# Performance work log

Hardware: AMD Instinct MI355X
Metric: run time of the kernel (lower is better)

## Reference

```python
import jax, jax.numpy as jnp
import numpy as np

D_MODEL = 512
N_HEADS = 8
D_FF = 2048
EPS = 1e-6


def layer_norm(x, g, b):
    mu = jnp.mean(x, axis=-1, keepdims=True)
    var = jnp.mean(jnp.square(x - mu), axis=-1, keepdims=True)
    return (x - mu) * jax.lax.rsqrt(var + EPS) * g + b


def setup_inputs() -> dict:
    key = jax.random.key(0)
    ks = jax.random.split(key, 6)
    B, S = 64, 500
    x = jax.random.normal(ks[0], (B, S, D_MODEL), dtype=jnp.float32)
    ln1_g = jnp.ones((D_MODEL,), jnp.float32)
    ln1_b = jnp.zeros((D_MODEL,), jnp.float32)
    ln2_g = jnp.ones((D_MODEL,), jnp.float32)
    ln2_b = jnp.zeros((D_MODEL,), jnp.float32)
    W1 = jax.random.normal(ks[1], (D_MODEL, D_FF), jnp.float32) * (1.0 / np.sqrt(D_MODEL))
    b1 = jnp.zeros((D_FF,), jnp.float32)
    W2 = jax.random.normal(ks[2], (D_FF, D_MODEL), jnp.float32) * (1.0 / np.sqrt(D_FF))
    b2 = jnp.zeros((D_MODEL,), jnp.float32)
    return {"x": x, "ln1_g": ln1_g, "ln1_b": ln1_b, "ln2_g": ln2_g, "ln2_b": ln2_b,
            "W1": W1, "b1": b1, "W2": W2, "b2": b2}


def causal_attention(h):
    # h: [B, S, D]; q=k=v=h (no projections in this module)
    B, S, D = h.shape
    Hd = D // N_HEADS
    qkv = h.reshape(B, S, N_HEADS, Hd).transpose(0, 2, 1, 3)  # [B, H, S, Hd]
    w = jnp.einsum('bhsd,bhtd->bhst', qkv, qkv) / jnp.sqrt(jnp.float32(Hd))
    mask = jnp.tril(jnp.ones((S, S), dtype=bool))
    w = jnp.where(mask, w, jnp.finfo(w.dtype).min)
    w = jax.nn.softmax(w, axis=-1)
    out = jnp.einsum('bhst,bhtd->bhsd', w, qkv)  # [B, H, S, Hd]
    return out.transpose(0, 2, 1, 3).reshape(B, S, D)


def reference(x, ln1_g, ln1_b, ln2_g, ln2_b, W1, b1, W2, b2):
    # Pre-LN block, but residuals attach to the post-LN activations (faithful to source).
    h = layer_norm(x, ln1_g, ln1_b)
    h = h + causal_attention(h)
    h2 = layer_norm(h, ln2_g, ln2_b)
    ff = jnp.maximum(h2 @ W1 + b1, 0.0) @ W2 + b2
    return h2 + ff
```

## Files before the change

kernel.cpp:

```cpp
#include <hip/hip_runtime.h>
#include <hip/hip_bf16.h>

#define D_MODEL 512
#define N_HEADS 8
#define HDIM 64
#define D_FF 2048
#define BATCH 64
#define SEQ 500
#define MROWS (BATCH * SEQ)

typedef __attribute__((ext_vector_type(8))) short bhalf8;
typedef __attribute__((ext_vector_type(4))) float floatx4;

#define AS_GLOBAL __attribute__((address_space(1)))
#define AS_LDS __attribute__((address_space(3)))

__device__ __forceinline__ void glds16(const void* g, void* l) {
  __builtin_amdgcn_global_load_lds((const AS_GLOBAL unsigned int*)g,
                                   (AS_LDS unsigned int*)l, 16, 0, 0);
}

__device__ __forceinline__ unsigned short f2bf(float f) {
  __hip_bfloat16 b = __float2bfloat16(f);
  return *reinterpret_cast<unsigned short*>(&b);
}

template <int MODE>
__global__ __launch_bounds__(256) void ln_kernel(const void* __restrict__ xin,
                                                 const float* __restrict__ g,
                                                 const float* __restrict__ b,
                                                 __hip_bfloat16* __restrict__ yb) {
  int row = blockIdx.x;
  int t = threadIdx.x;
  float v0, v1;
  if constexpr (MODE == 0) {
    float2 v = ((const float2*)xin)[(size_t)row * 256 + t];
    v0 = v.x; v1 = v.y;
  } else {
    __hip_bfloat162 bv = ((const __hip_bfloat162*)xin)[(size_t)row * 256 + t];
    v0 = __bfloat162float(bv.x); v1 = __bfloat162float(bv.y);
  }
  float s = v0 + v1;
  float sq = v0 * v0 + v1 * v1;
#pragma unroll
  for (int off = 32; off > 0; off >>= 1) {
    s += __shfl_down(s, off, 64);
    sq += __shfl_down(sq, off, 64);
  }
  __shared__ float red[8];
  if ((t & 63) == 0) {
    red[(t >> 6) * 2] = s;
    red[(t >> 6) * 2 + 1] = sq;
  }
  __syncthreads();
  s = red[0] + red[2] + red[4] + red[6];
  sq = red[1] + red[3] + red[5] + red[7];
  float mean = s * (1.0f / 512.0f);
  float var = sq * (1.0f / 512.0f) - mean * mean;
  float r = rsqrtf(var + 1e-6f);
  float2 gg = ((const float2*)g)[t];
  float2 bb = ((const float2*)b)[t];
  float y0 = (v0 - mean) * r * gg.x + bb.x;
  float y1 = (v1 - mean) * r * gg.y + bb.y;
  __hip_bfloat162 bv2;
  bv2.x = __float2bfloat16(y0);
  bv2.y = __float2bfloat16(y1);
  ((__hip_bfloat162*)yb)[(size_t)row * 256 + t] = bv2;
}

__global__ __launch_bounds__(256) void transpose_bf16(const float* __restrict__ W,
                                                      __hip_bfloat16* __restrict__ Wt,
                                                      int K, int N) {
  __shared__ float tile[32][33];
  int n0 = blockIdx.x * 32, k0 = blockIdx.y * 32;
  int tx = threadIdx.x, ty = threadIdx.y;
#pragma unroll
  for (int j = 0; j < 32; j += 8)
    tile[ty + j][tx] = W[(size_t)(k0 + ty + j) * N + n0 + tx];
  __syncthreads();
#pragma unroll
  for (int j = 0; j < 32; j += 8)
    Wt[(size_t)(n0 + ty + j) * K + k0 + tx] = __float2bfloat16(tile[tx][ty + j]);
}

__device__ __forceinline__ void attn_tile_step(int jq, int kt, int fr, int kg,
                                               const char* Kb, const char* Vb,
                                               char* Pw, bhalf8 (&qf)[2][2],
                                               floatx4 (&O)[2][4], float (&l)[2][4]) {
  int roff = 32 * jq - 64 * kt;
  bool domask = (jq <= 2 * kt + 1);
#pragma unroll
  for (int mr = 0; mr < 2; ++mr) {
    floatx4 S[4];
#pragma unroll
    for (int nc = 0; nc < 4; ++nc) S[nc] = (floatx4){0.f, 0.f, 0.f, 0.f};
    __builtin_amdgcn_s_setprio(1);
#pragma unroll
    for (int kk = 0; kk < 2; ++kk) {
#pragma unroll
      for (int nc = 0; nc < 4; ++nc) {
        bhalf8 kf = *(const bhalf8*)(Kb + (nc * 16 + fr) * 128 +
                                     (((kk * 4 + kg) ^ (fr & 7)) << 4));
        S[nc] = __builtin_amdgcn_mfma_f32_16x16x32_bf16(qf[mr][kk], kf, S[nc], 0, 0, 0);
      }
    }
    __builtin_amdgcn_s_setprio(0);
    if (domask) {
#pragma unroll
      for (int nc = 0; nc < 4; ++nc)
#pragma unroll
        for (int j = 0; j < 4; ++j)
          if (nc * 16 + fr > roff + mr * 16 + kg * 4 + j) S[nc][j] = -INFINITY;
    }
    float p[4][4];
#pragma unroll
    for (int nc = 0; nc < 4; ++nc)
#pragma unroll
      for (int j = 0; j < 4; ++j) {
        p[nc][j] = __expf(S[nc][j] * 0.125f - 66.0f);
        l[mr][j] += p[nc][j];
      }
#pragma unroll
    for (int nc = 0; nc < 4; ++nc)
#pragma unroll
      for (int j = 0; j < 4; ++j)
        *(unsigned short*)(Pw + ((kg * 4 + j) * 72 + nc * 16 + fr) * 2) = f2bf(p[nc][j]);
    __builtin_amdgcn_s_setprio(1);
#pragma unroll
    for (int kk = 0; kk < 2; ++kk) {
      bhalf8 pf = *(const bhalf8*)(Pw + fr * 144 + kk * 64 + kg * 16);
#pragma unroll
      for (int nc = 0; nc < 4; ++nc) {
        bhalf8 vf = *(const bhalf8*)(Vb + (nc * 16 + fr) * 144 + kk * 64 + kg * 16);
        O[mr][nc] = __builtin_amdgcn_mfma_f32_16x16x32_bf16(pf, vf, O[mr][nc], 0, 0, 0);
      }
    }
    __builtin_amdgcn_s_setprio(0);
  }
}

__global__ __launch_bounds__(512) void attn_fold(const __hip_bfloat16* __restrict__ hbp,
                                                 __hip_bfloat16* __restrict__ hres) {
  __shared__ unsigned short Ks[2][64 * 64];
  __shared__ unsigned short Vt[2][64 * 72];
  __shared__ unsigned short Ps[8][16 * 72];

  int blk = blockIdx.x;
  int b = blk >> 3, hd = blk & 7;
  int tid = threadIdx.x;
  int w = tid >> 6, lane = tid & 63;
  int fr = lane & 15, kg = lane >> 4;

  const unsigned short* hb = (const unsigned short*)hbp;
  size_t bbase = (size_t)b * SEQ * D_MODEL + hd * HDIM;

  int jH = 15 - w, jL = w;
  bhalf8 qH[2][2], qL[2][2];
#pragma unroll
  for (int mr = 0; mr < 2; ++mr) {
    int rH = 32 * jH + mr * 16 + fr;
    if (rH >= SEQ) rH = SEQ - 1;
    int rL = 32 * jL + mr * 16 + fr;
#pragma unroll
    for (int kk = 0; kk < 2; ++kk) {
      qH[mr][kk] = *(const bhalf8*)(hb + bbase + (size_t)rH * D_MODEL + kk * 32 + kg * 8);
      qL[mr][kk] = *(const bhalf8*)(hb + bbase + (size_t)rL * D_MODEL + kk * 32 + kg * 8);
    }
  }

  floatx4 OH[2][4], OL[2][4];
  float lHs[2][4], lLs[2][4];
#pragma unroll
  for (int mr = 0; mr < 2; ++mr)
#pragma unroll
    for (int nc = 0; nc < 4; ++nc) {
      OH[mr][nc] = (floatx4){0.f, 0.f, 0.f, 0.f};
      OL[mr][nc] = (floatx4){0.f, 0.f, 0.f, 0.f};
    }
#pragma unroll
  for (int mr = 0; mr < 2; ++mr)
#pragma unroll
    for (int j = 0; j < 4; ++j) { lHs[mr][j] = 0.f; lLs[mr][j] = 0.f; }

  int krow = w * 8 + (lane >> 3);
  int scb = (lane & 7) ^ (lane >> 3);

  {
    glds16(hb + bbase + (size_t)krow * D_MODEL + scb * 8, (char*)Ks[0] + w * 1024);
    bhalf8 v0 = *(const bhalf8*)(hb + bbase + (size_t)lane * D_MODEL + w * 8);
#pragma unroll
    for (int i = 0; i < 8; ++i) Vt[0][(w * 8 + i) * 72 + lane] = (unsigned short)v0[i];
  }
  __syncthreads();

  for (int kt = 0; kt < 8; ++kt) {
    int cur = kt & 1;
    bhalf8 vnext;
    if (kt < 7) {
      int sr = (kt + 1) * 64 + krow;
      if (sr >= SEQ) sr = SEQ - 1;
      glds16(hb + bbase + (size_t)sr * D_MODEL + scb * 8, (char*)Ks[cur ^ 1] + w * 1024);
      int vr = (kt + 1) * 64 + lane;
      if (vr >= SEQ) vr = SEQ - 1;
      vnext = *(const bhalf8*)(hb + bbase + (size_t)vr * D_MODEL + w * 8);
    }

    const char* Kb = (const char*)Ks[cur];
    const char* Vb = (const char*)Vt[cur];
    char* Pw = (char*)Ps[w];
    if (jH >= 2 * kt) attn_tile_step(jH, kt, fr, kg, Kb, Vb, Pw, qH, OH, lHs);
    if (jL >= 2 * kt) attn_tile_step(jL, kt, fr, kg, Kb, Vb, Pw, qL, OL, lLs);

    if (kt < 7) {
#pragma unroll
      for (int i = 0; i < 8; ++i)
        Vt[cur ^ 1][(w * 8 + i) * 72 + lane] = (unsigned short)vnext[i];
    }
    __syncthreads();
  }

#pragma unroll
  for (int off = 1; off < 16; off <<= 1)
#pragma unroll
    for (int mr = 0; mr < 2; ++mr)
#pragma unroll
      for (int j = 0; j < 4; ++j) {
        lHs[mr][j] += __shfl_xor(lHs[mr][j], off, 64);
        lLs[mr][j] += __shfl_xor(lLs[mr][j], off, 64);
      }

#pragma unroll
  for (int mr = 0; mr < 2; ++mr)
#pragma unroll
    for (int j = 0; j < 4; ++j) {
      int qH_row = 32 * jH + mr * 16 + kg * 4 + j;
      if (qH_row < SEQ) {
        float inv = 1.0f / lHs[mr][j];
        size_t ro = bbase + (size_t)qH_row * D_MODEL;
#pragma unroll
        for (int nc = 0; nc < 4; ++nc) {
          size_t idx = ro + nc * 16 + fr;
          float hv = __bfloat162float(hbp[idx]);
          hres[idx] = __float2bfloat16(hv + OH[mr][nc][j] * inv);
        }
      }
      int qL_row = 32 * jL + mr * 16 + kg * 4 + j;
      {
        float inv = 1.0f / lLs[mr][j];
        size_t ro = bbase + (size_t)qL_row * D_MODEL;
#pragma unroll
        for (int nc = 0; nc < 4; ++nc) {
          size_t idx = ro + nc * 16 + fr;
          float hv = __bfloat162float(hbp[idx]);
          hres[idx] = __float2bfloat16(hv + OL[mr][nc][j] * inv);
        }
      }
    }
}

template <int EPI>
__global__ __launch_bounds__(256, 4) void gemm97(const unsigned short* __restrict__ A,
                                                 const unsigned short* __restrict__ Bt,
                                                 const float* __restrict__ bias,
                                                 const __hip_bfloat16* __restrict__ resid,
                                                 float* __restrict__ outf,
                                                 __hip_bfloat16* __restrict__ outb,
                                                 int M, int N, int K, int gx) {
  __shared__ __align__(16) char smem[16384];

  int nwg = gridDim.x;
  int bid = blockIdx.x;
  int q = nwg >> 3, r = nwg & 7;
  int xcd = bid & 7, lo = bid >> 3;
  int wg = (xcd < r ? xcd * (q + 1) : r * (q + 1) + (xcd - r) * q) + lo;
  int by = wg / gx, bx = wg % gx;
  int m0 = by * 128, n0 = bx * 128;

  int tid = threadIdx.x;
  int w = tid >> 6, lane = tid & 63;
  int wr = (w >> 1) * 64, wc = (w & 1) * 64;
  int fr = lane & 15, kg = lane >> 4;

  int srow = lane >> 2;
  int scol = ((lane & 3) ^ ((lane >> 3) & 3)) * 8;
  const unsigned short* Ag0 = A + (size_t)(m0 + w * 16 + srow) * K + scol;
  const unsigned short* Ag1 = A + (size_t)(m0 + (w + 4) * 16 + srow) * K + scol;
  const unsigned short* Bg0 = Bt + (size_t)(n0 + w * 16 + srow) * K + scol;
  const unsigned short* Bg1 = Bt + (size_t)(n0 + (w + 4) * 16 + srow) * K + scol;
  char* dA0 = smem + w * 1024;
  char* dA1 = smem + (w + 4) * 1024;
  char* dB0 = smem + 8192 + w * 1024;
  char* dB1 = smem + 8192 + (w + 4) * 1024;

  int swz16 = (kg ^ ((fr >> 1) & 3)) << 4;
  const char* abase = smem + (wr + fr) * 64 + swz16;
  const char* bbase = smem + 8192 + (wc + fr) * 64 + swz16;

  floatx4 acc[4][4];
#pragma unroll
  for (int i = 0; i < 4; ++i)
#pragma unroll
    for (int j = 0; j < 4; ++j) acc[i][j] = (floatx4){0.f, 0.f, 0.f, 0.f};

  int nt = K >> 5;
  for (int t = 0; t < nt; ++t) {
    glds16(Ag0 + (size_t)t * 32, dA0);
    glds16(Ag1 + (size_t)t * 32, dA1);
    glds16(Bg0 + (size_t)t * 32, dB0);
    glds16(Bg1 + (size_t)t * 32, dB1);
    __syncthreads();

    bhalf8 av[4], bv[4];
#pragma unroll
    for (int mm = 0; mm < 4; ++mm) av[mm] = *(const bhalf8*)(abase + mm * 1024);
#pragma unroll
    for (int nn = 0; nn < 4; ++nn) bv[nn] = *(const bhalf8*)(bbase + nn * 1024);
#pragma unroll
    for (int mm = 0; mm < 4; ++mm)
#pragma unroll
      for (int nn = 0; nn < 4; ++nn)
        acc[mm][nn] =
            __builtin_amdgcn_mfma_f32_16x16x32_bf16(av[mm], bv[nn], acc[mm][nn], 0, 0, 0);
    __syncthreads();
  }

  int grow_base = m0 + wr + kg * 4;
  int gcol_base = n0 + wc + fr;
#pragma unroll
  for (int mm = 0; mm < 4; ++mm) {
#pragma unroll
    for (int nn = 0; nn < 4; ++nn) {
      int gc = gcol_base + nn * 16;
      float bi = bias[gc];
#pragma unroll
      for (int j = 0; j < 4; ++j) {
        int gr = grow_base + mm * 16 + j;
        float v = acc[mm][nn][j] + bi;
        size_t idx = (size_t)gr * N + gc;
        if (EPI == 1) {
          v = v > 0.f ? v : 0.f;
          outb[idx] = __float2bfloat16(v);
        } else {
          outf[idx] = __bfloat162float(resid[idx]) + v;
        }
      }
    }
  }
}

extern "C" void kernel_launch(void* const* d_in, const int* in_sizes, int n_in,
                              void* d_out, int out_size, void* d_ws, size_t ws_size,
                              hipStream_t stream) {
  const float* x = (const float*)d_in[0];
  const float* ln1g = (const float*)d_in[1];
  const float* ln1b = (const float*)d_in[2];
  const float* ln2g = (const float*)d_in[3];
  const float* ln2b = (const float*)d_in[4];
  const float* W1 = (const float*)d_in[5];
  const float* b1 = (const float*)d_in[6];
  const float* W2 = (const float*)d_in[7];
  const float* b2 = (const float*)d_in[8];
  float* out = (float*)d_out;

  char* ws = (char*)d_ws;
  __hip_bfloat16* h2b = (__hip_bfloat16*)ws;
  __hip_bfloat16* hb = (__hip_bfloat16*)(ws + 65536000);
  __hip_bfloat16* hresb = (__hip_bfloat16*)(ws + 98304000);
  __hip_bfloat16* u = (__hip_bfloat16*)(ws + 98304000);
  __hip_bfloat16* W1t = (__hip_bfloat16*)(ws + 229376000);
  __hip_bfloat16* W2t = (__hip_bfloat16*)(ws + 231473152);

  transpose_bf16<<<dim3(D_FF / 32, D_MODEL / 32), dim3(32, 8), 0, stream>>>(
      W1, W1t, D_MODEL, D_FF);
  transpose_bf16<<<dim3(D_MODEL / 32, D_FF / 32), dim3(32, 8), 0, stream>>>(
      W2, W2t, D_FF, D_MODEL);

  ln_kernel<0><<<MROWS, 256, 0, stream>>>(x, ln1g, ln1b, hb);

  attn_fold<<<BATCH * N_HEADS, 512, 0, stream>>>(hb, hresb);

  ln_kernel<1><<<MROWS, 256, 0, stream>>>(hresb, ln2g, ln2b, h2b);

  gemm97<1><<<(MROWS / 128) * (D_FF / 128), 256, 0, stream>>>(
      (const unsigned short*)h2b, (const unsigned short*)W1t, b1, nullptr,
      nullptr, u, MROWS, D_FF, D_MODEL, D_FF / 128);
  gemm97<2><<<(MROWS / 128) * (D_MODEL / 128), 256, 0, stream>>>(
      (const unsigned short*)u, (const unsigned short*)W2t, b2, h2b, out,
      nullptr, MROWS, D_MODEL, D_FF, D_MODEL / 128);
}
```

Before: 286.9 us.

## Double-buffer LDS tiles in GEMM to overlap global loads with MFMA

Doubles the GEMM's LDS to two 16KB buffers and prefetches the next K-tile via global_load_lds while the current tile is consumed by MFMAs. This drops one of the two barriers per iteration and adds s_setprio around the MFMA block so the compute waves get priority. The cost is twice the LDS per workgroup, which may limit occupancy under launch_bounds(256,4). Correctness depends on the single trailing barrier plus the vmcnt waits the compiler inserts around the async LDS loads.

```diff
diff --git a/kernel.cpp b/kernel.cpp
--- a/kernel.cpp
+++ b/kernel.cpp
@@ -266,7 +266,7 @@
                                                  float* __restrict__ outf,
                                                  __hip_bfloat16* __restrict__ outb,
                                                  int M, int N, int K, int gx) {
-  __shared__ __align__(16) char smem[16384];
+  __shared__ __align__(16) char smem[2 * 16384];
 
   int nwg = gridDim.x;
   int bid = blockIdx.x;
@@ -287,14 +287,12 @@
   const unsigned short* Ag1 = A + (size_t)(m0 + (w + 4) * 16 + srow) * K + scol;
   const unsigned short* Bg0 = Bt + (size_t)(n0 + w * 16 + srow) * K + scol;
   const unsigned short* Bg1 = Bt + (size_t)(n0 + (w + 4) * 16 + srow) * K + scol;
-  char* dA0 = smem + w * 1024;
-  char* dA1 = smem + (w + 4) * 1024;
-  char* dB0 = smem + 8192 + w * 1024;
-  char* dB1 = smem + 8192 + (w + 4) * 1024;
+  int dA0 = w * 1024, dA1 = (w + 4) * 1024;
+  int dB0 = 8192 + w * 1024, dB1 = 8192 + (w + 4) * 1024;
 
   int swz16 = (kg ^ ((fr >> 1) & 3)) << 4;
-  const char* abase = smem + (wr + fr) * 64 + swz16;
-  const char* bbase = smem + 8192 + (wc + fr) * 64 + swz16;
+  int aoff = (wr + fr) * 64 + swz16;
+  int boff = 8192 + (wc + fr) * 64 + swz16;
 
   floatx4 acc[4][4];
 #pragma unroll
@@ -303,26 +301,39 @@
     for (int j = 0; j < 4; ++j) acc[i][j] = (floatx4){0.f, 0.f, 0.f, 0.f};
 
   int nt = K >> 5;
+
+#define STAGE(t, buf)                                \
+  {                                                  \
+    char* d = smem + (buf) * 16384;                  \
+    glds16(Ag0 + (size_t)(t) * 32, d + dA0);         \
+    glds16(Ag1 + (size_t)(t) * 32, d + dA1);         \
+    glds16(Bg0 + (size_t)(t) * 32, d + dB0);         \
+    glds16(Bg1 + (size_t)(t) * 32, d + dB1);         \
+  }
+
+  STAGE(0, 0);
+  __syncthreads();
+
   for (int t = 0; t < nt; ++t) {
-    glds16(Ag0 + (size_t)t * 32, dA0);
-    glds16(Ag1 + (size_t)t * 32, dA1);
-    glds16(Bg0 + (size_t)t * 32, dB0);
-    glds16(Bg1 + (size_t)t * 32, dB1);
-    __syncthreads();
-
+    const char* bufp = smem + (t & 1) * 16384;
+    if (t + 1 < nt) STAGE(t + 1, (t + 1) & 1);
+    __builtin_amdgcn_sched_barrier(0);
     bhalf8 av[4], bv[4];
 #pragma unroll
-    for (int mm = 0; mm < 4; ++mm) av[mm] = *(const bhalf8*)(abase + mm * 1024);
-#pragma unroll
-    for (int nn = 0; nn < 4; ++nn) bv[nn] = *(const bhalf8*)(bbase + nn * 1024);
+    for (int mm = 0; mm < 4; ++mm) av[mm] = *(const bhalf8*)(bufp + aoff + mm * 1024);
+#pragma unroll
+    for (int nn = 0; nn < 4; ++nn) bv[nn] = *(const bhalf8*)(bufp + boff + nn * 1024);
+    __builtin_amdgcn_s_setprio(1);
 #pragma unroll
     for (int mm = 0; mm < 4; ++mm)
 #pragma unroll
       for (int nn = 0; nn < 4; ++nn)
         acc[mm][nn] =
             __builtin_amdgcn_mfma_f32_16x16x32_bf16(av[mm], bv[nn], acc[mm][nn], 0, 0, 0);
+    __builtin_amdgcn_s_setprio(0);
     __syncthreads();
   }
+#undef STAGE
 
   int grow_base = m0 + wr + kg * 4;
   int gcol_base = n0 + wc + fr;
```

Measured after the change: 289.5 us. About the same (+0.9%).
